# Performance work log

Measured on AMD Instinct MI355X. Metric: run time of the kernel, lower is better.

## Reference

```python
import jax, jax.numpy as jnp
import numpy as np

B, S, HID, H = 4, 4096, 1024, 16
EPS = 1e-12  # F.normalize default eps


def setup_inputs() -> dict:
    key = jax.random.key(0)
    ks = jax.random.split(key, 3)
    def lin_w(k, shape, fan_in):
        return jax.random.normal(k, shape, jnp.float32) * (fan_in ** -0.5)
    return {
        "x": jax.random.normal(ks[0], (B, S, HID), jnp.float32),
        "Wqkv": lin_w(ks[1], (3 * HID, HID), HID),
        "bqkv": jnp.zeros((3 * HID,), jnp.float32),
        "Wz": lin_w(ks[2], (HID, HID), HID),
        "bz": jnp.zeros((HID,), jnp.float32),
        "temperature": jnp.ones((H, 1, 1), jnp.float32),
    }


def reference(x, Wqkv, bqkv, Wz, bz, temperature):
    b, s, hid = x.shape
    h = temperature.shape[0]
    dh = hid // h
    scale = jnp.sqrt(jnp.asarray(hid, x.dtype))
    # QKV projection -> [3, B, H, Dh, S] (channels-as-tokens layout)
    qkv = (x @ Wqkv.T + bqkv).reshape(b, s, 3, h, dh)
    qkv = jnp.transpose(qkv, (2, 0, 3, 4, 1))
    Q, K, V = qkv[0], qkv[1], qkv[2]
    # L2-normalize along sequence axis (last dim)
    Q = Q / jnp.maximum(jnp.linalg.norm(Q, axis=-1, keepdims=True), EPS)
    K = K / jnp.maximum(jnp.linalg.norm(K, axis=-1, keepdims=True), EPS)
    # Channel-channel scores [B, H, Dh, Dh], temperature broadcasts per head
    w = jnp.einsum('bhds,bhes->bhde', Q, K) / scale * temperature
    attn = jax.nn.softmax(w, axis=-1)
    out = jnp.einsum('bhde,bhes->bhds', attn, V)  # [B, H, Dh, S]
    out = jnp.transpose(out, (0, 3, 1, 2)).reshape(b, s, hid)
    return out @ Wz.T + bz
```

## Files before the change

kernel.cpp:

```cpp
#include <hip/hip_runtime.h>

#define DEVINL __device__ __forceinline__

#define BB 4
#define SS 4096
#define HIDD 1024
#define HH 16
#define DH 64
#define NQKV 3072
#define MM (BB * SS)

typedef __attribute__((ext_vector_type(8))) short bf16x8_t;
typedef __attribute__((ext_vector_type(4))) float f32x4_t;

typedef __attribute__((address_space(1))) const void GV;
typedef __attribute__((address_space(3))) void LV;

DEVINL void gload16(const void* g, void* l) {
  __builtin_amdgcn_global_load_lds((GV*)g, (LV*)l, 16, 0, 0);
}

DEVINL float bf2f(ushort u) {
  union { unsigned int i; float f; } v;
  v.i = ((unsigned int)u) << 16;
  return v.f;
}
DEVINL ushort f2bf(float f) {
  unsigned int u = __float_as_uint(f);
  u = (u + 0x7fffu + ((u >> 16) & 1u)) >> 16;
  return (ushort)u;
}

__global__ __launch_bounds__(256) void k_f2bf(const float* __restrict__ src,
                                              ushort* __restrict__ dst, int n4) {
  int i = blockIdx.x * 256 + threadIdx.x;
  if (i >= n4) return;
  float4 v = ((const float4*)src)[i];
  ushort4 o;
  o.x = f2bf(v.x); o.y = f2bf(v.y); o.z = f2bf(v.z); o.w = f2bf(v.w);
  ((ushort4*)dst)[i] = o;
}

template <int MODE>
__global__ __launch_bounds__(512, 2) void k_gemm8p(
    const ushort* __restrict__ A, const ushort* __restrict__ B,
    const float* __restrict__ bias, void* __restrict__ Cv,
    ushort* __restrict__ qT, ushort* __restrict__ vbuf,
    int M, int N, int K) {
  __shared__ ushort As0[256 * 64];
  __shared__ ushort As1[256 * 64];
  __shared__ ushort Bs0[256 * 64];
  __shared__ ushort Bs1[256 * 64];
  __shared__ ushort Dmy[4096];
  const int t = threadIdx.x;
  const int m0 = blockIdx.x * 256, n0 = blockIdx.y * 256;
  const int lane = t & 63, wid = t >> 6;
  const int wm = wid >> 2, wn = wid & 3;
  const int fr = lane & 15, g = lane >> 4;
  const int srow = t >> 3;
  const int schunk = ((t & 7) ^ (srow & 7)) * 8;
  const int NT = K >> 6;
  const ushort* Ag = A + (size_t)m0 * K;
  const ushort* Bg = B + (size_t)n0 * K;

  f32x4_t acc[8][4] = {};
  bf16x8_t af[2][2], bfr[4][2];

#define STG(ls_, gsrc, tile, hf)                                            \
  {                                                                         \
    if ((tile) < NT) {                                                      \
      const ushort* gs_ = (gsrc) + (size_t)((hf) * 128 + srow) * K +        \
                          (tile) * 64 + schunk;                             \
      ushort* ld_ = (ls_) + ((hf) * 128 + wid * 8) * 64;                    \
      gload16(gs_, ld_);                                                    \
      gload16(gs_ + (size_t)64 * K, ld_ + 64 * 64);                         \
    } else {                                                                \
      const ushort* gs_ = (gsrc) + (size_t)srow * K + schunk;               \
      ushort* ld_ = Dmy + wid * 512;                                        \
      gload16(gs_, ld_);                                                    \
      gload16(gs_, ld_);                                                    \
    }                                                                       \
  }

#define LDA(as_, q)                                                         \
  _Pragma("unroll") for (int ii = 0; ii < 2; ++ii)                          \
  _Pragma("unroll") for (int kk = 0; kk < 2; ++kk) {                        \
    int r = wm * 128 + ((q) * 2 + ii) * 16 + fr;                            \
    af[ii][kk] = *(const bf16x8_t*)&(as_)[r * 64 + (((kk * 4 + g) ^ (r & 7)) * 8)]; \
  }

#define LDB(bs_)                                                            \
  _Pragma("unroll") for (int ni = 0; ni < 4; ++ni)                          \
  _Pragma("unroll") for (int kk = 0; kk < 2; ++kk) {                        \
    int r = wn * 64 + ni * 16 + fr;                                         \
    bfr[ni][kk] = *(const bf16x8_t*)&(bs_)[r * 64 + (((kk * 4 + g) ^ (r & 7)) * 8)]; \
  }

#define MMA(q)                                                              \
  _Pragma("unroll") for (int kk = 0; kk < 2; ++kk)                          \
  _Pragma("unroll") for (int ii = 0; ii < 2; ++ii)                          \
  _Pragma("unroll") for (int ni = 0; ni < 4; ++ni)                          \
    acc[(q) * 2 + ii][ni] = __builtin_amdgcn_mfma_f32_16x16x32_bf16(        \
        af[ii][kk], bfr[ni][kk], acc[(q) * 2 + ii][ni], 0, 0, 0);

#define BAR1                                                                \
  __builtin_amdgcn_s_barrier();                                             \
  asm volatile("s_waitcnt lgkmcnt(0)" ::: "memory");                        \
  __builtin_amdgcn_sched_barrier(0);                                        \
  __builtin_amdgcn_s_setprio(1);

#define BAR2                                                                \
  __builtin_amdgcn_s_setprio(0);                                            \
  __builtin_amdgcn_s_barrier();                                             \
  __builtin_amdgcn_sched_barrier(0);

#define BAR2VM                                                              \
  __builtin_amdgcn_s_setprio(0);                                            \
  asm volatile("s_waitcnt vmcnt(4)" ::: "memory");                          \
  __builtin_amdgcn_s_barrier();                                             \
  __builtin_amdgcn_sched_barrier(0);

  STG(Bs0, Bg, 0, 0); STG(Bs0, Bg, 0, 1);
  STG(As0, Ag, 0, 0); STG(As0, Ag, 0, 1);
  STG(Bs1, Bg, 1, 0); STG(Bs1, Bg, 1, 1);
  asm volatile("s_waitcnt vmcnt(4)" ::: "memory");
  __builtin_amdgcn_s_barrier();
  __builtin_amdgcn_sched_barrier(0);

  for (int J = 0; J < (NT >> 1); ++J) {
    const int T0 = 2 * J, T1 = 2 * J + 1;
    LDA(As0, 0); LDB(Bs0); STG(As1, Ag, T1, 0);
    BAR1; MMA(0); BAR2;
    LDA(As0, 1); STG(As1, Ag, T1, 1);
    BAR1; MMA(1); BAR2;
    LDA(As0, 2); STG(Bs0, Bg, T0 + 2, 0);
    BAR1; MMA(2); BAR2;
    LDA(As0, 3); STG(Bs0, Bg, T0 + 2, 1);
    BAR1; MMA(3); BAR2VM;
    LDA(As1, 0); LDB(Bs1); STG(As0, Ag, T0 + 2, 0);
    BAR1; MMA(0); BAR2;
    LDA(As1, 1); STG(As0, Ag, T0 + 2, 1);
    BAR1; MMA(1); BAR2;
    LDA(As1, 2); STG(Bs1, Bg, T1 + 2, 0);
    BAR1; MMA(2); BAR2;
    LDA(As1, 3); STG(Bs1, Bg, T1 + 2, 1);
    BAR1; MMA(3); BAR2VM;
  }
#undef STG
#undef LDA
#undef LDB
#undef MMA
#undef BAR1
#undef BAR2
#undef BAR2VM

#pragma unroll
  for (int ni = 0; ni < 4; ++ni) {
    int col = n0 + wn * 64 + ni * 16 + fr;
    float bv = bias[col];
#pragma unroll
    for (int mi = 0; mi < 8; ++mi) {
      int rowbase = m0 + wm * 128 + mi * 16 + g * 4;
      if (MODE == 1) {
#pragma unroll
        for (int j = 0; j < 4; ++j)
          ((float*)Cv)[(size_t)(rowbase + j) * N + col] = acc[mi][ni][j] + bv;
      } else {
        ushort4 o;
        o.x = f2bf(acc[mi][ni][0] + bv);
        o.y = f2bf(acc[mi][ni][1] + bv);
        o.z = f2bf(acc[mi][ni][2] + bv);
        o.w = f2bf(acc[mi][ni][3] + bv);
        if (col < 2048) {
          int tt = col >> 10;
          int hh = (col >> 6) & 15;
          int d = col & 63;
          int b = rowbase >> 12;
          int s = rowbase & 4095;
          size_t off = ((((size_t)tt * BB + b) * HH + hh) * 64 + d) * SS + s;
          *(ushort4*)&qT[off] = o;
        } else {
          int c = col - 2048;
          vbuf[(size_t)(rowbase + 0) * HIDD + c] = o.x;
          vbuf[(size_t)(rowbase + 1) * HIDD + c] = o.y;
          vbuf[(size_t)(rowbase + 2) * HIDD + c] = o.z;
          vbuf[(size_t)(rowbase + 3) * HIDD + c] = o.w;
        }
      }
    }
  }
}

__global__ __launch_bounds__(256) void k_norms(const ushort* __restrict__ qT,
                                               float* __restrict__ invq,
                                               float* __restrict__ invk) {
  int wave = threadIdx.x >> 6, lane = threadIdx.x & 63;
  int row = blockIdx.x * 4 + wave;
  const ushort* src = qT + (size_t)row * SS;
  float s = 0.f;
#pragma unroll
  for (int c = 0; c < 8; ++c) {
    bf16x8_t v = *(const bf16x8_t*)&src[c * 512 + lane * 8];
#pragma unroll
    for (int j = 0; j < 8; ++j) {
      float f = bf2f((ushort)v[j]);
      s += f * f;
    }
  }
#pragma unroll
  for (int off = 32; off; off >>= 1) s += __shfl_xor(s, off, 64);
  if (lane == 0) {
    float inv = 1.0f / fmaxf(sqrtf(s), 1e-12f);
    if (row < 4096) invq[row] = inv;
    else invk[row - 4096] = inv;
  }
}

__global__ __launch_bounds__(256) void k_gram(const ushort* __restrict__ qT,
                                              float* __restrict__ Wpart) {
  __shared__ ushort Qs[64 * 64];
  __shared__ ushort Ks[64 * 64];
  int bh = blockIdx.x, p = blockIdx.y;
  const ushort* Qp = qT + (size_t)bh * 64 * SS + p * 1024;
  const ushort* Kp = qT + (size_t)(BB * HH + bh) * 64 * SS + p * 1024;
  const int t = threadIdx.x;
  const int lane = t & 63, w = t >> 6;
  const int fr = lane & 15, g = lane >> 4;
  const int rsub = lane >> 3;
  const int gcol = ((lane & 7) ^ rsub) * 8;
  f32x4_t acc[4] = {};
  for (int sc = 0; sc < 16; ++sc) {
#pragma unroll
    for (int i = 0; i < 2; ++i) {
      int rg = w * 2 + i;
      int row = rg * 8 + rsub;
      gload16(&Qp[(size_t)row * SS + sc * 64 + gcol], &Qs[rg * 512]);
      gload16(&Kp[(size_t)row * SS + sc * 64 + gcol], &Ks[rg * 512]);
    }
    __syncthreads();
#pragma unroll
    for (int kk = 0; kk < 2; ++kk) {
      int r = w * 16 + fr;
      bf16x8_t af = *(const bf16x8_t*)&Qs[r * 64 + (((kk * 4 + g) ^ (r & 7)) * 8)];
#pragma unroll
      for (int ni = 0; ni < 4; ++ni) {
        int r2 = ni * 16 + fr;
        bf16x8_t bfg = *(const bf16x8_t*)&Ks[r2 * 64 + (((kk * 4 + g) ^ (r2 & 7)) * 8)];
        acc[ni] = __builtin_amdgcn_mfma_f32_16x16x32_bf16(af, bfg, acc[ni], 0, 0, 0);
      }
    }
    __syncthreads();
  }
  float* wp = Wpart + (size_t)(bh * 4 + p) * 4096;
#pragma unroll
  for (int ni = 0; ni < 4; ++ni)
#pragma unroll
    for (int j = 0; j < 4; ++j)
      wp[(w * 16 + g * 4 + j) * 64 + ni * 16 + fr] = acc[ni][j];
}

__global__ __launch_bounds__(256) void k_pv(const ushort* __restrict__ vbuf,
                                            const float* __restrict__ Wpart,
                                            const float* __restrict__ invq,
                                            const float* __restrict__ invk,
                                            const float* __restrict__ temperature,
                                            ushort* __restrict__ attnout) {
  __shared__ float attnf[64][65];
  __shared__ ushort attnb[64 * 72];
  __shared__ ushort Vs[64 * 64];
  int bh = blockIdx.x, p = blockIdx.y;
  int b = bh >> 4, h = bh & 15;
  const int t = threadIdx.x;
  const int lane = t & 63, w = t >> 6;
  const int fr = lane & 15, g = lane >> 4;
  const int rsub = lane >> 3;
  const int gcol = ((lane & 7) ^ rsub) * 8;
  float tscale = temperature[h] * (1.0f / 32.0f);
  for (int idx = t; idx < 4096; idx += 256) {
    int d = idx >> 6, e = idx & 63;
    float s = 0.f;
#pragma unroll
    for (int q = 0; q < 4; ++q) s += Wpart[(size_t)(bh * 4 + q) * 4096 + idx];
    attnf[d][e] = s * invq[bh * 64 + d] * invk[bh * 64 + e] * tscale;
  }
  __syncthreads();
  if (t < 64) {
    float m = -1e30f;
#pragma unroll 8
    for (int e = 0; e < 64; ++e) m = fmaxf(m, attnf[t][e]);
    float sum = 0.f;
#pragma unroll 8
    for (int e = 0; e < 64; ++e) {
      float v = __expf(attnf[t][e] - m);
      attnf[t][e] = v;
      sum += v;
    }
    float inv = 1.0f / sum;
#pragma unroll 8
    for (int e = 0; e < 64; ++e) attnb[t * 72 + e] = f2bf(attnf[t][e] * inv);
  }
  __syncthreads();
  bf16x8_t bfg[4][2];
#pragma unroll
  for (int ni = 0; ni < 4; ++ni)
#pragma unroll
    for (int kk = 0; kk < 2; ++kk)
      bfg[ni][kk] = *(const bf16x8_t*)&attnb[(ni * 16 + fr) * 72 + (kk * 4 + g) * 8];

  const ushort* vb = vbuf + (size_t)(b * SS + p * 1024) * HIDD + h * 64;
  ushort* ob = attnout + (size_t)(b * SS + p * 1024) * HIDD + h * 64;
  for (int s0 = 0; s0 < 1024; s0 += 64) {
#pragma unroll
    for (int i = 0; i < 2; ++i) {
      int rg = w * 2 + i;
      int row = rg * 8 + rsub;
      gload16(&vb[(size_t)(s0 + row) * HIDD + gcol], &Vs[rg * 512]);
    }
    __syncthreads();
    f32x4_t acc[4] = {};
#pragma unroll
    for (int kk = 0; kk < 2; ++kk) {
      int r = w * 16 + fr;
      bf16x8_t af = *(const bf16x8_t*)&Vs[r * 64 + (((kk * 4 + g) ^ (r & 7)) * 8)];
#pragma unroll
      for (int ni = 0; ni < 4; ++ni)
        acc[ni] = __builtin_amdgcn_mfma_f32_16x16x32_bf16(af, bfg[ni][kk], acc[ni], 0, 0, 0);
    }
#pragma unroll
    for (int ni = 0; ni < 4; ++ni)
#pragma unroll
      for (int j = 0; j < 4; ++j)
        ob[(size_t)(s0 + w * 16 + g * 4 + j) * HIDD + ni * 16 + fr] = f2bf(acc[ni][j]);
    __syncthreads();
  }
}

extern "C" void kernel_launch(void* const* d_in, const int* in_sizes, int n_in,
                              void* d_out, int out_size, void* d_ws, size_t ws_size,
                              hipStream_t stream) {
  const float* x = (const float*)d_in[0];
  const float* Wqkv = (const float*)d_in[1];
  const float* bqkv = (const float*)d_in[2];
  const float* Wz = (const float*)d_in[3];
  const float* bz = (const float*)d_in[4];
  const float* temperature = (const float*)d_in[5];

  char* ws = (char*)d_ws;
  ushort* xb   = (ushort*)(ws + 0);
  ushort* wqb  = (ushort*)(ws + 33554432);
  ushort* wzb  = (ushort*)(ws + 39845888);
  ushort* vbuf = (ushort*)(ws + 41943040);
  ushort* qkvT = (ushort*)(ws + 75497472);
  float* invq  = (float*)(ws + 142606336);
  float* invk  = (float*)(ws + 142622720);
  float* Wpart = (float*)(ws + 142639104);
  ushort* attnout = xb;

  k_f2bf<<<dim3(16384), dim3(256), 0, stream>>>(x, xb, (MM * HIDD) / 4);
  k_f2bf<<<dim3(3072), dim3(256), 0, stream>>>(Wqkv, wqb, (NQKV * HIDD) / 4);
  k_f2bf<<<dim3(1024), dim3(256), 0, stream>>>(Wz, wzb, (HIDD * HIDD) / 4);

  k_gemm8p<2><<<dim3(MM / 256, NQKV / 256), dim3(512), 0, stream>>>(
      xb, wqb, bqkv, nullptr, qkvT, vbuf, MM, NQKV, HIDD);

  k_gram<<<dim3(64, 4), dim3(256), 0, stream>>>(qkvT, Wpart);
  k_norms<<<dim3(2048), dim3(256), 0, stream>>>(qkvT, invq, invk);

  k_pv<<<dim3(64, 4), dim3(256), 0, stream>>>(vbuf, Wpart, invq, invk, temperature,
                                              attnout);

  k_gemm8p<1><<<dim3(MM / 256, HIDD / 256), dim3(512), 0, stream>>>(
      attnout, wzb, bz, d_out, nullptr, nullptr, MM, HIDD, HIDD);
}
```

Measured before the change: 238.1 us.

## Fuse L2 norms and softmax into a pipelined single-pass Gram kernel

Replaces the separate k_gram and k_norms kernels and the softmax prologue of k_pv with one kernel per (batch, head). It walks the whole sequence through a triple-buffered async LDS pipeline and accumulates squared norms from the same loaded fragments. Softmax is done in registers with shuffles, and k_pv receives a ready bf16 attention matrix. This removes the second read of Q/K and the partial-sum round trip, and saves a launch. In exchange the Gram stage drops from 256 blocks to 64. Separately, the explicit lgkmcnt wait and sched barriers in the GEMM barrier macros are dropped, leaving LDS wait placement to the compiler.

Result: slower. 677.6 us (+184.5%).

```diff
diff --git a/kernel.cpp b/kernel.cpp
--- a/kernel.cpp
+++ b/kernel.cpp
@@ -105,14 +105,11 @@
 
 #define BAR1                                                                \
   __builtin_amdgcn_s_barrier();                                             \
-  asm volatile("s_waitcnt lgkmcnt(0)" ::: "memory");                        \
-  __builtin_amdgcn_sched_barrier(0);                                        \
   __builtin_amdgcn_s_setprio(1);
 
 #define BAR2                                                                \
   __builtin_amdgcn_s_setprio(0);                                            \
-  __builtin_amdgcn_s_barrier();                                             \
-  __builtin_amdgcn_sched_barrier(0);
+  __builtin_amdgcn_s_barrier();
 
 #define BAR2VM                                                              \
   __builtin_amdgcn_s_setprio(0);                                            \
@@ -191,82 +188,117 @@
   }
 }
 
-__global__ __launch_bounds__(256) void k_norms(const ushort* __restrict__ qT,
-                                               float* __restrict__ invq,
-                                               float* __restrict__ invk) {
-  int wave = threadIdx.x >> 6, lane = threadIdx.x & 63;
-  int row = blockIdx.x * 4 + wave;
-  const ushort* src = qT + (size_t)row * SS;
-  float s = 0.f;
-#pragma unroll
-  for (int c = 0; c < 8; ++c) {
-    bf16x8_t v = *(const bf16x8_t*)&src[c * 512 + lane * 8];
-#pragma unroll
-    for (int j = 0; j < 8; ++j) {
-      float f = bf2f((ushort)v[j]);
-      s += f * f;
-    }
-  }
-#pragma unroll
-  for (int off = 32; off; off >>= 1) s += __shfl_xor(s, off, 64);
-  if (lane == 0) {
-    float inv = 1.0f / fmaxf(sqrtf(s), 1e-12f);
-    if (row < 4096) invq[row] = inv;
-    else invk[row - 4096] = inv;
-  }
-}
-
-__global__ __launch_bounds__(256) void k_gram(const ushort* __restrict__ qT,
-                                              float* __restrict__ Wpart) {
-  __shared__ ushort Qs[64 * 64];
-  __shared__ ushort Ks[64 * 64];
-  int bh = blockIdx.x, p = blockIdx.y;
-  const ushort* Qp = qT + (size_t)bh * 64 * SS + p * 1024;
-  const ushort* Kp = qT + (size_t)(BB * HH + bh) * 64 * SS + p * 1024;
+__global__ __launch_bounds__(256) void k_gram_sm(const ushort* __restrict__ qT,
+                                                 const float* __restrict__ temperature,
+                                                 ushort* __restrict__ attnb) {
+  __shared__ ushort Qs[3][64 * 64];
+  __shared__ ushort Ks[3][64 * 64];
+  __shared__ ushort dmy[2048];
+  __shared__ float sql[64], skl[64];
+  const int bh = blockIdx.x, h = bh & 15;
+  const ushort* Qp = qT + (size_t)bh * 64 * SS;
+  const ushort* Kp = qT + (size_t)(BB * HH + bh) * 64 * SS;
   const int t = threadIdx.x;
   const int lane = t & 63, w = t >> 6;
   const int fr = lane & 15, g = lane >> 4;
   const int rsub = lane >> 3;
   const int gcol = ((lane & 7) ^ rsub) * 8;
+
   f32x4_t acc[4] = {};
-  for (int sc = 0; sc < 16; ++sc) {
-#pragma unroll
-    for (int i = 0; i < 2; ++i) {
-      int rg = w * 2 + i;
-      int row = rg * 8 + rsub;
-      gload16(&Qp[(size_t)row * SS + sc * 64 + gcol], &Qs[rg * 512]);
-      gload16(&Kp[(size_t)row * SS + sc * 64 + gcol], &Ks[rg * 512]);
-    }
-    __syncthreads();
+  float sqa = 0.f, ska = 0.f;
+
+#define STGG(b_, sc_)                                                       \
+  _Pragma("unroll") for (int i = 0; i < 2; ++i) {                           \
+    int rg = w * 2 + i;                                                     \
+    int row = rg * 8 + rsub;                                                \
+    gload16(&Qp[(size_t)row * SS + (sc_) * 64 + gcol], &Qs[b_][rg * 512]);  \
+    gload16(&Kp[(size_t)row * SS + (sc_) * 64 + gcol], &Ks[b_][rg * 512]);  \
+  }
+
+  STGG(0, 0);
+  STGG(1, 1);
+  for (int sc = 0; sc < 64; ++sc) {
+    if (sc + 2 < 64) {
+      int b2 = (sc + 2) % 3;
+      STGG(b2, sc + 2);
+    } else {
+#pragma unroll
+      for (int i = 0; i < 2; ++i) {
+        gload16(&Qp[(size_t)rsub * SS + gcol], &dmy[w * 512]);
+        gload16(&Kp[(size_t)rsub * SS + gcol], &dmy[w * 512]);
+      }
+    }
+    asm volatile("s_waitcnt vmcnt(8)" ::: "memory");
+    __builtin_amdgcn_s_barrier();
+    __builtin_amdgcn_sched_barrier(0);
+    const int bc = sc % 3;
+    bf16x8_t af[2], bq[4][2];
 #pragma unroll
     for (int kk = 0; kk < 2; ++kk) {
       int r = w * 16 + fr;
-      bf16x8_t af = *(const bf16x8_t*)&Qs[r * 64 + (((kk * 4 + g) ^ (r & 7)) * 8)];
-#pragma unroll
-      for (int ni = 0; ni < 4; ++ni) {
+      af[kk] = *(const bf16x8_t*)&Qs[bc][r * 64 + (((kk * 4 + g) ^ (r & 7)) * 8)];
+    }
+#pragma unroll
+    for (int ni = 0; ni < 4; ++ni)
+#pragma unroll
+      for (int kk = 0; kk < 2; ++kk) {
         int r2 = ni * 16 + fr;
-        bf16x8_t bfg = *(const bf16x8_t*)&Ks[r2 * 64 + (((kk * 4 + g) ^ (r2 & 7)) * 8)];
-        acc[ni] = __builtin_amdgcn_mfma_f32_16x16x32_bf16(af, bfg, acc[ni], 0, 0, 0);
+        bq[ni][kk] = *(const bf16x8_t*)&Ks[bc][r2 * 64 + (((kk * 4 + g) ^ (r2 & 7)) * 8)];
       }
-    }
-    __syncthreads();
-  }
-  float* wp = Wpart + (size_t)(bh * 4 + p) * 4096;
+#pragma unroll
+    for (int kk = 0; kk < 2; ++kk)
+#pragma unroll
+      for (int ni = 0; ni < 4; ++ni)
+        acc[ni] = __builtin_amdgcn_mfma_f32_16x16x32_bf16(af[kk], bq[ni][kk], acc[ni], 0, 0, 0);
+#pragma unroll
+    for (int kk = 0; kk < 2; ++kk)
+#pragma unroll
+      for (int e = 0; e < 8; ++e) {
+        float fq = bf2f((ushort)af[kk][e]);
+        sqa += fq * fq;
+        float fk = bf2f((ushort)bq[w][kk][e]);
+        ska += fk * fk;
+      }
+    __builtin_amdgcn_s_barrier();
+    __builtin_amdgcn_sched_barrier(0);
+  }
+#undef STGG
+
+  sqa += __shfl_xor(sqa, 16, 64); sqa += __shfl_xor(sqa, 32, 64);
+  ska += __shfl_xor(ska, 16, 64); ska += __shfl_xor(ska, 32, 64);
+  if (g == 0) { sql[w * 16 + fr] = sqa; skl[w * 16 + fr] = ska; }
+  __syncthreads();
+
+  float tscale = temperature[h] * (1.0f / 32.0f);
+  float ik[4];
 #pragma unroll
   for (int ni = 0; ni < 4; ++ni)
-#pragma unroll
-    for (int j = 0; j < 4; ++j)
-      wp[(w * 16 + g * 4 + j) * 64 + ni * 16 + fr] = acc[ni][j];
+    ik[ni] = 1.0f / fmaxf(sqrtf(skl[ni * 16 + fr]), 1e-12f);
+#pragma unroll
+  for (int j = 0; j < 4; ++j) {
+    int row = w * 16 + g * 4 + j;
+    float iq = 1.0f / fmaxf(sqrtf(sql[row]), 1e-12f);
+    float v[4];
+#pragma unroll
+    for (int ni = 0; ni < 4; ++ni) v[ni] = acc[ni][j] * iq * ik[ni] * tscale;
+    float m = fmaxf(fmaxf(v[0], v[1]), fmaxf(v[2], v[3]));
+#pragma unroll
+    for (int off = 1; off < 16; off <<= 1) m = fmaxf(m, __shfl_xor(m, off, 64));
+    float p[4], s = 0.f;
+#pragma unroll
+    for (int ni = 0; ni < 4; ++ni) { p[ni] = __expf(v[ni] - m); s += p[ni]; }
+#pragma unroll
+    for (int off = 1; off < 16; off <<= 1) s += __shfl_xor(s, off, 64);
+    float inv = 1.0f / s;
+#pragma unroll
+    for (int ni = 0; ni < 4; ++ni)
+      attnb[(size_t)bh * 4608 + row * 72 + ni * 16 + fr] = f2bf(p[ni] * inv);
+  }
 }
 
 __global__ __launch_bounds__(256) void k_pv(const ushort* __restrict__ vbuf,
-                                            const float* __restrict__ Wpart,
-                                            const float* __restrict__ invq,
-                                            const float* __restrict__ invk,
-                                            const float* __restrict__ temperature,
+                                            const ushort* __restrict__ attnb,
                                             ushort* __restrict__ attnout) {
-  __shared__ float attnf[64][65];
-  __shared__ ushort attnb[64 * 72];
   __shared__ ushort Vs[64 * 64];
   int bh = blockIdx.x, p = blockIdx.y;
   int b = bh >> 4, h = bh & 15;
@@ -275,37 +307,13 @@
   const int fr = lane & 15, g = lane >> 4;
   const int rsub = lane >> 3;
   const int gcol = ((lane & 7) ^ rsub) * 8;
-  float tscale = temperature[h] * (1.0f / 32.0f);
-  for (int idx = t; idx < 4096; idx += 256) {
-    int d = idx >> 6, e = idx & 63;
-    float s = 0.f;
-#pragma unroll
-    for (int q = 0; q < 4; ++q) s += Wpart[(size_t)(bh * 4 + q) * 4096 + idx];
-    attnf[d][e] = s * invq[bh * 64 + d] * invk[bh * 64 + e] * tscale;
-  }
-  __syncthreads();
-  if (t < 64) {
-    float m = -1e30f;
-#pragma unroll 8
-    for (int e = 0; e < 64; ++e) m = fmaxf(m, attnf[t][e]);
-    float sum = 0.f;
-#pragma unroll 8
-    for (int e = 0; e < 64; ++e) {
-      float v = __expf(attnf[t][e] - m);
-      attnf[t][e] = v;
-      sum += v;
-    }
-    float inv = 1.0f / sum;
-#pragma unroll 8
-    for (int e = 0; e < 64; ++e) attnb[t * 72 + e] = f2bf(attnf[t][e] * inv);
-  }
-  __syncthreads();
+
   bf16x8_t bfg[4][2];
 #pragma unroll
   for (int ni = 0; ni < 4; ++ni)
 #pragma unroll
     for (int kk = 0; kk < 2; ++kk)
-      bfg[ni][kk] = *(const bf16x8_t*)&attnb[(ni * 16 + fr) * 72 + (kk * 4 + g) * 8];
+      bfg[ni][kk] = *(const bf16x8_t*)&attnb[(size_t)bh * 4608 + (ni * 16 + fr) * 72 + (kk * 4 + g) * 8];
 
   const ushort* vb = vbuf + (size_t)(b * SS + p * 1024) * HIDD + h * 64;
   ushort* ob = attnout + (size_t)(b * SS + p * 1024) * HIDD + h * 64;
@@ -346,14 +354,12 @@
   const float* temperature = (const float*)d_in[5];
 
   char* ws = (char*)d_ws;
-  ushort* xb   = (ushort*)(ws + 0);
-  ushort* wqb  = (ushort*)(ws + 33554432);
-  ushort* wzb  = (ushort*)(ws + 39845888);
-  ushort* vbuf = (ushort*)(ws + 41943040);
-  ushort* qkvT = (ushort*)(ws + 75497472);
-  float* invq  = (float*)(ws + 142606336);
-  float* invk  = (float*)(ws + 142622720);
-  float* Wpart = (float*)(ws + 142639104);
+  ushort* xb    = (ushort*)(ws + 0);
+  ushort* wqb   = (ushort*)(ws + 33554432);
+  ushort* wzb   = (ushort*)(ws + 39845888);
+  ushort* vbuf  = (ushort*)(ws + 41943040);
+  ushort* qkvT  = (ushort*)(ws + 75497472);
+  ushort* attnb = (ushort*)(ws + 142639104);
   ushort* attnout = xb;
 
   k_f2bf<<<dim3(16384), dim3(256), 0, stream>>>(x, xb, (MM * HIDD) / 4);
@@ -363,11 +369,9 @@
   k_gemm8p<2><<<dim3(MM / 256, NQKV / 256), dim3(512), 0, stream>>>(
       xb, wqb, bqkv, nullptr, qkvT, vbuf, MM, NQKV, HIDD);
 
-  k_gram<<<dim3(64, 4), dim3(256), 0, stream>>>(qkvT, Wpart);
-  k_norms<<<dim3(2048), dim3(256), 0, stream>>>(qkvT, invq, invk);
-
-  k_pv<<<dim3(64, 4), dim3(256), 0, stream>>>(vbuf, Wpart, invq, invk, temperature,
-                                              attnout);
+  k_gram_sm<<<dim3(64), dim3(256), 0, stream>>>(qkvT, temperature, attnb);
+
+  k_pv<<<dim3(64, 4), dim3(256), 0, stream>>>(vbuf, attnb, attnout);
 
   k_gemm8p<1><<<dim3(MM / 256, HIDD / 256), dim3(512), 0, stream>>>(
       attnout, wzb, bz, d_out, nullptr, nullptr, MM, HIDD, HIDD);
```
